# Optimization experiments

Measured on AMD Instinct MI355X. Metric: run time of the kernel, lower is better.

The kernel has to match this reference:

```python
import jax, jax.numpy as jnp
import numpy as np

B, C_IN, C_OUT, H, W, K, STRIDE, PAD = 16, 64, 64, 256, 256, 3, 1, 1


def setup_inputs() -> dict:
    key = jax.random.key(0)
    k_x, k_w, k_b = jax.random.split(key, 3)
    x = jax.random.normal(k_x, (B, C_IN, H, W), dtype=jnp.float32)
    # kaiming_normal fan_out init: std = sqrt(2 / (C_OUT * K * K))
    std = float(np.sqrt(2.0 / (C_OUT * K * K)))
    weight = jax.random.normal(k_w, (C_OUT, C_IN, K, K), dtype=jnp.float32) * std
    bias = jnp.zeros((C_OUT,), dtype=jnp.float32)
    return {"x": x, "weight": weight, "bias": bias}


def reference(x, weight, bias):
    # The torch module computes an offset via offset_conv but never uses it;
    # the nested-loop unfold+weighted-sum is mathematically a plain conv2d.
    out = jax.lax.conv_general_dilated(
        x, weight,
        window_strides=(STRIDE, STRIDE),
        padding=[(PAD, PAD), (PAD, PAD)],
        dimension_numbers=("NCHW", "OIHW", "NCHW"),
    )
    return out + bias[None, :, None, None]
```

## Files before the change

### kernel.cpp

```cpp
#include <hip/hip_runtime.h>
#include <hip/hip_bf16.h>

#define HWX 65536u
#define ROWS 18
#define RCELLS 34

typedef __attribute__((ext_vector_type(8)))  __bf16 bf16x8;
typedef __attribute__((ext_vector_type(16))) float  f32x16;

__device__ __forceinline__ unsigned pk2(float lo, float hi) {
    __hip_bfloat162 p = __float22bfloat162_rn(make_float2(lo, hi));
    union { __hip_bfloat162 b; unsigned u; } v; v.b = p; return v.u;
}

__global__ void prep_weights(const float* __restrict__ wgt,
                             unsigned short* __restrict__ wsA) {
    int idx = blockIdx.x * 256 + threadIdx.x;
    if (idx >= 9 * 64 * 64) return;
    int j    = idx & 7;
    int co   = (idx >> 3) & 63;
    int rest = idx >> 9;
    int h = rest & 1, kc = (rest >> 1) & 3, tap = rest >> 3;
    int ci = kc * 16 + h * 8 + j;
    __hip_bfloat16 b = __float2bfloat16(wgt[(co * 64 + ci) * 9 + tap]);
    union { __hip_bfloat16 b; unsigned short s; } v; v.b = b;
    wsA[idx] = v.s;
}

__global__ __launch_bounds__(512, 4) void conv_mfma(
    const float* __restrict__ x, const unsigned short* __restrict__ wsA_in,
    const float* __restrict__ bias, float* __restrict__ out)
{
    __shared__ __align__(16) char s_in[ROWS * RCELLS * 128];

    const int t    = threadIdx.x;
    const int l    = t & 63;
    const int wave = t >> 6;
    const int n    = l & 31;
    const int h    = l >> 5;
    const int co0  = (wave & 1) * 32;
    const int wrow = (wave >> 1) * 4;

    const int bid   = (int)blockIdx.x;
    const int xh    = bid & 1;
    const int strip = (bid >> 1) & 15;
    const int b     = bid >> 5;
    const int y0    = strip * 16;

    const int cp  = t >> 4;
    const int ixp = t & 15;

    const float* xp0 = x + (size_t)(b * 64 + cp * 2) * HWX;

    for (int i = 0; i < 4; ++i) {
        const int x0 = (xh * 4 + i) * 32;

        #pragma unroll 6
        for (int iy = 0; iy < ROWS; ++iy) {
            const int gy = y0 + iy - 1;
            float2 a = make_float2(0.f, 0.f), c = make_float2(0.f, 0.f);
            if ((unsigned)gy < 256u) {
                const float* p = xp0 + (unsigned)gy * 256u + (unsigned)(x0 + ixp * 2);
                a = *(const float2*)p;
                c = *(const float2*)(p + HWX);
            }
            const int ix0 = ixp * 2 + 1;
            unsigned base = (unsigned)((iy * RCELLS + ix0) * 128);
            unsigned o0 = base + ((((cp >> 2) ^ (ix0 & 7)) << 4) | ((cp & 3) << 2));
            unsigned o1 = base + 128 + ((((cp >> 2) ^ ((ix0 + 1) & 7)) << 4) | ((cp & 3) << 2));
            *(unsigned*)(s_in + o0) = pk2(a.x, c.x);
            *(unsigned*)(s_in + o1) = pk2(a.y, c.y);
        }
        #pragma unroll
        for (int it = 0; it < 3; ++it) {
            int id = t + it * 512;
            if (id < 1152) {
                int col = (id >= 576) ? 1 : 0;
                int r   = id - col * 576;
                int iy  = r >> 5;
                int cq  = r & 31;
                int gx  = col ? x0 + 32 : x0 - 1;
                int gy  = y0 + iy - 1;
                float f0 = 0.f, f1 = 0.f;
                if (((unsigned)gy < 256u) && ((unsigned)gx < 256u)) {
                    const float* q = x + (size_t)(b * 64 + cq * 2) * HWX
                                   + (unsigned)gy * 256u + (unsigned)gx;
                    f0 = q[0]; f1 = q[HWX];
                }
                int ix = col ? 33 : 0;
                unsigned off = (unsigned)((iy * RCELLS + ix) * 128)
                             + ((((cq >> 2) ^ (ix & 7)) << 4) | ((cq & 3) << 2));
                *(unsigned*)(s_in + off) = pk2(f0, f1);
            }
        }
        __syncthreads();

        const unsigned short* wp0 = wsA_in;

        f32x16 acc[4];
        #pragma unroll
        for (int r = 0; r < 4; ++r) acc[r] = (f32x16)0.0f;

        #pragma unroll 1
        for (int dx = 0; dx < 3; ++dx) {
            const unsigned short* wp = wp0;
            asm volatile("" : "+s"(wp));
            #pragma unroll
            for (int kc = 0; kc < 4; ++kc) {
                bf16x8 af[3];
                #pragma unroll
                for (int dy = 0; dy < 3; ++dy) {
                    const int tap = dy * 3 + dx;
                    af[dy] = *(const bf16x8*)(wp +
                        ((((tap * 4 + kc) * 2 + h) * 64 + co0 + n) * 8));
                }
                #pragma unroll
                for (int iyo = 0; iyo < 6; ++iyo) {
                    const int iy = wrow + iyo;
                    const int ix = n + dx;
                    const bf16x8 bf = *(const bf16x8*)(s_in
                        + (iy * RCELLS + ix) * 128 + (((kc * 2 + h) ^ (ix & 7)) << 4));
                    #pragma unroll
                    for (int dy = 0; dy < 3; ++dy) {
                        const int r = iyo - dy;
                        if (r >= 0 && r < 4)
                            acc[r] = __builtin_amdgcn_mfma_f32_32x32x16_bf16(
                                af[dy], bf, acc[r], 0, 0, 0);
                    }
                }
            }
        }
        __syncthreads();

        const unsigned obase = (unsigned)(b * 64) * HWX + (unsigned)(x0 + n);
        #pragma unroll
        for (int reg = 0; reg < 16; ++reg) {
            const int row = (reg & 3) + 8 * (reg >> 2) + 4 * h;
            const float bb = bias[co0 + row];
            const unsigned cb = obase + (unsigned)(co0 + row) * HWX;
            #pragma unroll
            for (int r = 0; r < 4; ++r) {
                const unsigned Y = (unsigned)(y0 + wrow + r);
                out[cb + Y * 256u] = acc[r][reg] + bb;
            }
        }
    }
}

extern "C" void kernel_launch(void* const* d_in, const int* in_sizes, int n_in,
                              void* d_out, int out_size, void* d_ws, size_t ws_size,
                              hipStream_t stream) {
    const float* x    = (const float*)d_in[0];
    const float* wgt  = (const float*)d_in[1];
    const float* bias = (const float*)d_in[2];
    float* out = (float*)d_out;
    unsigned short* wsA = (unsigned short*)d_ws;

    prep_weights<<<dim3(144), dim3(256), 0, stream>>>(wgt, wsA);
    conv_mfma<<<dim3(512), dim3(512), 0, stream>>>(x, wsA, bias, out);
}
```

Baseline: 528.2 us.

## Double-buffer input tiles with register prefetch across full-row strips

Adds a second LDS input buffer and issues the global loads for the next 32-column tile into registers before the MFMA loop, writing them to the other buffer afterward. Memory latency is meant to overlap with compute instead of stalling before each tile. Each block now covers a whole row strip (8 tiles) with half the grid, plus a remapped block index. The cost is 36 extra VGPRs of staging state, launch bounds lowered to 2 blocks/SM, doubled LDS, and only 256 blocks, which may underfill the GPU's 256 CUs.

```diff
diff --git a/kernel.cpp b/kernel.cpp
--- a/kernel.cpp
+++ b/kernel.cpp
@@ -4,6 +4,7 @@
 #define HWX 65536u
 #define ROWS 18
 #define RCELLS 34
+#define BUFB (ROWS * RCELLS * 128)
 
 typedef __attribute__((ext_vector_type(8)))  __bf16 bf16x8;
 typedef __attribute__((ext_vector_type(16))) float  f32x16;
@@ -27,11 +28,75 @@
     wsA[idx] = v.s;
 }
 
-__global__ __launch_bounds__(512, 4) void conv_mfma(
+struct StageRegs {
+    float2 a[ROWS], c[ROWS];
+    float  f0[3], f1[3];
+};
+
+__device__ __forceinline__ void stage_issue(StageRegs& S, const float* __restrict__ x,
+                                            int b, int cp, int ixp, int t, int y0, int x0) {
+    const float* xp0 = x + (size_t)(b * 64 + cp * 2) * HWX + (unsigned)(x0 + ixp * 2);
+    #pragma unroll
+    for (int iy = 0; iy < ROWS; ++iy) {
+        const int gy = y0 + iy - 1;
+        S.a[iy] = make_float2(0.f, 0.f);
+        S.c[iy] = make_float2(0.f, 0.f);
+        if ((unsigned)gy < 256u) {
+            const float* p = xp0 + (unsigned)gy * 256u;
+            S.a[iy] = *(const float2*)p;
+            S.c[iy] = *(const float2*)(p + HWX);
+        }
+    }
+    #pragma unroll
+    for (int it = 0; it < 3; ++it) {
+        const int id = t + it * 512;
+        S.f0[it] = 0.f; S.f1[it] = 0.f;
+        if (id < 1152) {
+            const int col = (id >= 576) ? 1 : 0;
+            const int r   = id - col * 576;
+            const int iy  = r >> 5, cq = r & 31;
+            const int gx  = col ? x0 + 32 : x0 - 1;
+            const int gy  = y0 + iy - 1;
+            if (((unsigned)gy < 256u) && ((unsigned)gx < 256u)) {
+                const float* q = x + (size_t)(b * 64 + cq * 2) * HWX
+                               + (unsigned)gy * 256u + (unsigned)gx;
+                S.f0[it] = q[0]; S.f1[it] = q[HWX];
+            }
+        }
+    }
+}
+
+__device__ __forceinline__ void stage_consume(const StageRegs& S, char* wr,
+                                              int cp, int ixp, int t) {
+    #pragma unroll
+    for (int iy = 0; iy < ROWS; ++iy) {
+        const int ix0 = ixp * 2 + 1;
+        unsigned base = (unsigned)((iy * RCELLS + ix0) * 128);
+        unsigned o0 = base + ((((cp >> 2) ^ (ix0 & 7)) << 4) | ((cp & 3) << 2));
+        unsigned o1 = base + 128 + ((((cp >> 2) ^ ((ix0 + 1) & 7)) << 4) | ((cp & 3) << 2));
+        *(unsigned*)(wr + o0) = pk2(S.a[iy].x, S.c[iy].x);
+        *(unsigned*)(wr + o1) = pk2(S.a[iy].y, S.c[iy].y);
+    }
+    #pragma unroll
+    for (int it = 0; it < 3; ++it) {
+        const int id = t + it * 512;
+        if (id < 1152) {
+            const int col = (id >= 576) ? 1 : 0;
+            const int r   = id - col * 576;
+            const int iy  = r >> 5, cq = r & 31;
+            const int ix  = col ? 33 : 0;
+            unsigned off = (unsigned)((iy * RCELLS + ix) * 128)
+                         + ((((cq >> 2) ^ (ix & 7)) << 4) | ((cq & 3) << 2));
+            *(unsigned*)(wr + off) = pk2(S.f0[it], S.f1[it]);
+        }
+    }
+}
+
+__global__ __launch_bounds__(512, 2) void conv_mfma(
     const float* __restrict__ x, const unsigned short* __restrict__ wsA_in,
     const float* __restrict__ bias, float* __restrict__ out)
 {
-    __shared__ __align__(16) char s_in[ROWS * RCELLS * 128];
+    __shared__ __align__(16) char s_in[2 * BUFB];
 
     const int t    = threadIdx.x;
     const int l    = t & 63;
@@ -41,59 +106,27 @@
     const int co0  = (wave & 1) * 32;
     const int wrow = (wave >> 1) * 4;
 
-    const int bid   = (int)blockIdx.x;
-    const int xh    = bid & 1;
-    const int strip = (bid >> 1) & 15;
-    const int b     = bid >> 5;
+    const int bid0 = (int)blockIdx.x;
+    const int bid  = (bid0 & 7) * 32 + (bid0 >> 3);
+    const int strip = bid & 15;
+    const int b     = bid >> 4;
     const int y0    = strip * 16;
 
     const int cp  = t >> 4;
     const int ixp = t & 15;
 
-    const float* xp0 = x + (size_t)(b * 64 + cp * 2) * HWX;
+    StageRegs S;
+    stage_issue(S, x, b, cp, ixp, t, y0, 0);
+    stage_consume(S, s_in, cp, ixp, t);
+    __syncthreads();
 
-    for (int i = 0; i < 4; ++i) {
-        const int x0 = (xh * 4 + i) * 32;
+    #pragma unroll 1
+    for (int i = 0; i < 8; ++i) {
+        const int x0 = i * 32;
+        const char* rd = s_in + (i & 1) * BUFB;
+        char*       wr = s_in + ((i + 1) & 1) * BUFB;
 
-        #pragma unroll 6
-        for (int iy = 0; iy < ROWS; ++iy) {
-            const int gy = y0 + iy - 1;
-            float2 a = make_float2(0.f, 0.f), c = make_float2(0.f, 0.f);
-            if ((unsigned)gy < 256u) {
-                const float* p = xp0 + (unsigned)gy * 256u + (unsigned)(x0 + ixp * 2);
-                a = *(const float2*)p;
-                c = *(const float2*)(p + HWX);
-            }
-            const int ix0 = ixp * 2 + 1;
-            unsigned base = (unsigned)((iy * RCELLS + ix0) * 128);
-            unsigned o0 = base + ((((cp >> 2) ^ (ix0 & 7)) << 4) | ((cp & 3) << 2));
-            unsigned o1 = base + 128 + ((((cp >> 2) ^ ((ix0 + 1) & 7)) << 4) | ((cp & 3) << 2));
-            *(unsigned*)(s_in + o0) = pk2(a.x, c.x);
-            *(unsigned*)(s_in + o1) = pk2(a.y, c.y);
-        }
-        #pragma unroll
-        for (int it = 0; it < 3; ++it) {
-            int id = t + it * 512;
-            if (id < 1152) {
-                int col = (id >= 576) ? 1 : 0;
-                int r   = id - col * 576;
-                int iy  = r >> 5;
-                int cq  = r & 31;
-                int gx  = col ? x0 + 32 : x0 - 1;
-                int gy  = y0 + iy - 1;
-                float f0 = 0.f, f1 = 0.f;
-                if (((unsigned)gy < 256u) && ((unsigned)gx < 256u)) {
-                    const float* q = x + (size_t)(b * 64 + cq * 2) * HWX
-                                   + (unsigned)gy * 256u + (unsigned)gx;
-                    f0 = q[0]; f1 = q[HWX];
-                }
-                int ix = col ? 33 : 0;
-                unsigned off = (unsigned)((iy * RCELLS + ix) * 128)
-                             + ((((cq >> 2) ^ (ix & 7)) << 4) | ((cq & 3) << 2));
-                *(unsigned*)(s_in + off) = pk2(f0, f1);
-            }
-        }
-        __syncthreads();
+        if (i < 7) stage_issue(S, x, b, cp, ixp, t, y0, x0 + 32);
 
         const unsigned short* wp0 = wsA_in;
 
@@ -118,7 +151,7 @@
                 for (int iyo = 0; iyo < 6; ++iyo) {
                     const int iy = wrow + iyo;
                     const int ix = n + dx;
-                    const bf16x8 bf = *(const bf16x8*)(s_in
+                    const bf16x8 bf = *(const bf16x8*)(rd
                         + (iy * RCELLS + ix) * 128 + (((kc * 2 + h) ^ (ix & 7)) << 4));
                     #pragma unroll
                     for (int dy = 0; dy < 3; ++dy) {
@@ -130,6 +163,8 @@
                 }
             }
         }
+
+        if (i < 7) stage_consume(S, wr, cp, ixp, t);
         __syncthreads();
 
         const unsigned obase = (unsigned)(b * 64) * HWX + (unsigned)(x0 + n);
@@ -157,5 +192,5 @@
     unsigned short* wsA = (unsigned short*)d_ws;
 
     prep_weights<<<dim3(144), dim3(256), 0, stream>>>(wgt, wsA);
-    conv_mfma<<<dim3(512), dim3(512), 0, stream>>>(x, wsA, bias, out);
+    conv_mfma<<<dim3(256), dim3(512), 0, stream>>>(x, wsA, bias, out);
 }
```

Result: no change. 525.4 us (-0.5%).
